# Kernel tuning notes

Hardware: AMD Instinct MI355X
Metric: run time of the kernel (lower is better)

The kernel has to match this reference:

```python
import jax, jax.numpy as jnp
import numpy as np

N_FFT = 1024
HOP = 256
B = 8
T = 2048  # n_frames
FREQ = N_FFT // 2 + 1


def setup_inputs() -> dict:
    key = jax.random.key(0)
    k1, k2 = jax.random.split(key)
    real_stft = jax.random.normal(k1, (B, 1, T, FREQ), dtype=jnp.float32)
    imag_stft = jax.random.normal(k2, (B, 1, T, FREQ), dtype=jnp.float32)
    # Build DFT synthesis matrices (same as torch module __init__, scaled=False)
    n = np.arange(N_FFT)
    hann = (0.5 - 0.5 * np.cos(2.0 * np.pi * n / N_FFT))  # fftbins=True hann
    ang = 2.0 * np.pi * np.outer(n, n) / N_FFT            # [k, n]
    W_real = (np.cos(ang) * hann[None, :] / N_FFT).astype(np.float32)
    W_imag = (np.sin(ang) * hann[None, :] / N_FFT).astype(np.float32)
    ola_window = (hann ** 2).astype(np.float32)
    return {
        "real_stft": real_stft,
        "imag_stft": imag_stft,
        "W_real": jnp.asarray(W_real),
        "W_imag": jnp.asarray(W_imag),
        "ola_window": jnp.asarray(ola_window),
    }


def reference(real_stft, imag_stft, W_real, W_imag, ola_window):
    n_fft = W_real.shape[0]
    b, _, n_frames, _ = real_stft.shape
    # (B, T, F) -> (B, F, T)
    fr = jnp.swapaxes(real_stft[:, 0], 1, 2)
    fi = jnp.swapaxes(imag_stft[:, 0], 1, 2)
    # Hermitian extension to full spectrum (B, n_fft, T)
    full_r = jnp.concatenate([fr, jnp.flip(fr[:, 1:-1, :], axis=1)], axis=1)
    full_i = jnp.concatenate([fi, -jnp.flip(fi[:, 1:-1, :], axis=1)], axis=1)
    # 1x1-conv DFT projection: out[b,t,n] = sum_k W[k,n] * x[b,k,t]
    frames = (jnp.einsum('kn,bkt->btn', W_real, full_r)
              - jnp.einsum('kn,bkt->btn', W_imag, full_i))  # (B, T, n_fft)
    out_len = (n_frames - 1) * HOP + n_fft
    # Overlap-add fold via scatter-add
    idx = (jnp.arange(n_frames)[:, None] * HOP + jnp.arange(n_fft)[None, :]).reshape(-1)
    y = jnp.zeros((b, out_len), frames.dtype).at[:, idx].add(frames.reshape(b, -1))
    # Window-sum fold + normalization
    wsum = jnp.zeros((out_len,), frames.dtype).at[idx].add(jnp.tile(ola_window, n_frames))
    wsum = jnp.clip(wsum, 1e-11, None)
    y = y / wsum[None, :]
    half = n_fft // 2
    return y[:, half:out_len - half]
```

## Files before the change

kernel.cpp:

```cpp
#include <hip/hip_runtime.h>


#define BATCH    8
#define NFRAMES  2048
#define FREQ     513
#define OUTCOLS  524032
#define FRAMES_B ((size_t)16384 * 1024 * 2)
#define WS_NEED  FRAMES_B

typedef __attribute__((ext_vector_type(2))) float f32x2;
typedef __attribute__((ext_vector_type(4))) float f32x4;
typedef __attribute__((ext_vector_type(4))) unsigned uint4v;

__device__ __forceinline__ unsigned short f2bf(float x) {
    unsigned u = __float_as_uint(x);
    return (unsigned short)((u + 0x7fffu + ((u >> 16) & 1u)) >> 16);
}

#define DSYNC() do { asm volatile("s_waitcnt lgkmcnt(0)" ::: "memory"); \
                     __builtin_amdgcn_sched_barrier(0); } while (0)

#define BFLY(IA, IB, IC, ID, T1, O0, O1, O2, O3)                              \
    {                                                                         \
        f32x2 apc = (IA) + (IC), amc = (IA) - (IC);                           \
        f32x2 bpd = (IB) + (ID), bmd = (IB) - (ID);                           \
        f32x2 jb  = (f32x2){-bmd[1], bmd[0]};                    \
        float rev_ = (float)(T1) * (1.0f / 1024.0f);                          \
        float s1_ = __builtin_amdgcn_sinf(rev_);                              \
        float c1_ = __builtin_amdgcn_cosf(rev_);                              \
        float c2_ = fmaf(-2.0f * s1_, s1_, 1.0f), s2_ = 2.0f * s1_ * c1_;     \
        float c3_ = c2_ * c1_ - s2_ * s1_, s3_ = s2_ * c1_ + c2_ * s1_;       \
        f32x2 u1 = amc + jb, u2 = apc - bpd, u3 = amc - jb;                   \
        O0 = apc + bpd;                                                       \
        O1 = (f32x2){u1[0] * c1_ - u1[1] * s1_, u1[0] * s1_ + u1[1] * c1_};   \
        O2 = (f32x2){u2[0] * c2_ - u2[1] * s2_, u2[0] * s2_ + u2[1] * c2_};   \
        O3 = (f32x2){u3[0] * c3_ - u3[1] * s3_, u3[0] * s3_ + u3[1] * c3_};   \
    }

__global__ __launch_bounds__(256, 2) void ifft_wave5(
    const float* __restrict__ re, const float* __restrict__ im,
    const float* __restrict__ ola, unsigned short* __restrict__ frames) {
    __shared__ float LR[4][1052];
    __shared__ float LI[4][1052];

    const int tid = threadIdx.x;
    const int l   = tid & 63;
    const int w   = tid >> 6;
    const int r0  = (blockIdx.x * 4 + w) * 2;
    float* PR = &LR[w][0];
    float* PI = &LI[w][0];

    const float* fre0 = re + (size_t)r0 * FREQ;
    const float* fim0 = im + (size_t)r0 * FREQ;
    const float* fre1 = fre0 + FREQ;
    const float* fim1 = fim0 + FREQ;

    f32x2 s1v[4][4];
#pragma unroll
    for (int j = 0; j < 4; ++j) {
        f32x2 in[4];
#pragma unroll
        for (int k = 0; k < 4; ++k) {
            int n  = l + 64 * j + 256 * k;
            int mm = (n <= 512) ? n : (1024 - n);
            float A1 = fre0[mm], B1 = fim0[mm];
            float A2 = fre1[mm], B2 = fim1[mm];
            if (n == 0 || n == 512) { B1 = 0.0f; B2 = 0.0f; }
            in[k] = (n <= 512) ? (f32x2){A1 - B2, B1 + A2}
                               : (f32x2){A1 + B2, A2 - B1};
        }
        BFLY(in[0], in[1], in[2], in[3], l + 64 * j,
             s1v[j][0], s1v[j][1], s1v[j][2], s1v[j][3]);
    }

    f32x4 wRe[4], wIm[4];
#pragma unroll
    for (int r = 0; r < 4; ++r) {
        f32x2 o0, o1, o2, o3;
        BFLY(s1v[0][r], s1v[1][r], s1v[2][r], s1v[3][r], 4 * l, o0, o1, o2, o3);
        wRe[0][r] = o0[0]; wIm[0][r] = o0[1];
        wRe[1][r] = o1[0]; wIm[1][r] = o1[1];
        wRe[2][r] = o2[0]; wIm[2][r] = o2[1];
        wRe[3][r] = o3[0]; wIm[3][r] = o3[1];
    }

    {
        const int wb = 16 * l + 8 * (l >> 4);
#pragma unroll
        for (int k = 0; k < 4; ++k) *(f32x4*)&PR[wb + 4 * k] = wRe[k];
#pragma unroll
        for (int k = 0; k < 4; ++k) *(f32x4*)&PI[wb + 4 * k] = wIm[k];
    }
    DSYNC();
    float rr[4][4], ri[4][4];
#pragma unroll
    for (int j = 0; j < 4; ++j)
#pragma unroll
        for (int k = 0; k < 4; ++k) rr[j][k] = PR[l + 64 * j + 264 * k];
#pragma unroll
    for (int j = 0; j < 4; ++j)
#pragma unroll
        for (int k = 0; k < 4; ++k) ri[j][k] = PI[l + 64 * j + 264 * k];

    f32x2 s3v[4][4];
#pragma unroll
    for (int j = 0; j < 4; ++j) {
        f32x2 a = (f32x2){rr[j][0], ri[j][0]};
        f32x2 b = (f32x2){rr[j][1], ri[j][1]};
        f32x2 c = (f32x2){rr[j][2], ri[j][2]};
        f32x2 d = (f32x2){rr[j][3], ri[j][3]};
        BFLY(a, b, c, d, (((l + 64 * j) >> 4) << 4),
             s3v[j][0], s3v[j][1], s3v[j][2], s3v[j][3]);
    }

    float eRe[4][4], eIm[4][4];
#pragma unroll
    for (int r = 0; r < 4; ++r) {
        f32x2 o0, o1, o2, o3;
        BFLY(s3v[0][r], s3v[1][r], s3v[2][r], s3v[3][r], ((l >> 4) << 6),
             o0, o1, o2, o3);
        eRe[0][r] = o0[0]; eIm[0][r] = o0[1];
        eRe[1][r] = o1[0]; eIm[1][r] = o1[1];
        eRe[2][r] = o2[0]; eIm[2][r] = o2[1];
        eRe[3][r] = o3[0]; eIm[3][r] = o3[1];
    }

    DSYNC();
    {
        const int wb = 256 * (l >> 4) + (l & 15) + 8 * (l >> 4);
#pragma unroll
        for (int k = 0; k < 4; ++k)
#pragma unroll
            for (int r = 0; r < 4; ++r) PR[wb + 16 * r + 64 * k] = eRe[k][r];
#pragma unroll
        for (int k = 0; k < 4; ++k)
#pragma unroll
            for (int r = 0; r < 4; ++r) PI[wb + 16 * r + 64 * k] = eIm[k][r];
    }
    DSYNC();
    float yR[4][4], yI[4][4];
#pragma unroll
    for (int h = 0; h < 4; ++h)
#pragma unroll
        for (int k = 0; k < 4; ++k) yR[h][k] = PR[l + 64 * h + 264 * k];
#pragma unroll
    for (int h = 0; h < 4; ++h)
#pragma unroll
        for (int k = 0; k < 4; ++k) yI[h][k] = PI[l + 64 * h + 264 * k];

    unsigned short* fR = frames + (size_t)r0 * 1024;
    unsigned short* fI = fR + 1024;
#pragma unroll
    for (int h = 0; h < 4; ++h) {
        f32x2 a = (f32x2){yR[h][0], yI[h][0]};
        f32x2 b = (f32x2){yR[h][1], yI[h][1]};
        f32x2 c = (f32x2){yR[h][2], yI[h][2]};
        f32x2 d = (f32x2){yR[h][3], yI[h][3]};
        f32x2 apc = a + c, amc = a - c, bpd = b + d, bmd = b - d;
        f32x2 jb  = (f32x2){-bmd[1], bmd[0]};
        f32x2 y0 = apc + bpd, y1 = amc + jb, y2 = apc - bpd, y3 = amc - jb;
        int n0 = l + 64 * h;
        float h0 = sqrtf(ola[n0])       * (1.0f / 1024.0f);
        float h1 = sqrtf(ola[n0 + 256]) * (1.0f / 1024.0f);
        float h2 = sqrtf(ola[n0 + 512]) * (1.0f / 1024.0f);
        float h3 = sqrtf(ola[n0 + 768]) * (1.0f / 1024.0f);
        fR[n0]       = f2bf(y0[0] * h0);  fI[n0]       = f2bf(y0[1] * h0);
        fR[n0 + 256] = f2bf(y1[0] * h1);  fI[n0 + 256] = f2bf(y1[1] * h1);
        fR[n0 + 512] = f2bf(y2[0] * h2);  fI[n0 + 512] = f2bf(y2[1] * h2);
        fR[n0 + 768] = f2bf(y3[0] * h3);  fI[n0 + 768] = f2bf(y3[1] * h3);
    }
}

__global__ __launch_bounds__(256) void ola_fold8(
    const unsigned short* __restrict__ frames, const float* __restrict__ ola,
    float* __restrict__ out) {
    const int col0 = (blockIdx.x * 256 + threadIdx.x) * 8;
    if (col0 >= OUTCOLS) return;
    const int b  = blockIdx.y;
    const int s  = col0 + 512;
    const int g  = s >> 8;
    const int ls = s & 255;

    float acc[8] = {0.f, 0.f, 0.f, 0.f, 0.f, 0.f, 0.f, 0.f};
    float wsm[8] = {0.f, 0.f, 0.f, 0.f, 0.f, 0.f, 0.f, 0.f};
#pragma unroll
    for (int j = 0; j < 4; ++j) {
        const int t = g - j;
        if (t >= 0 && t < NFRAMES) {
            uint4v u = *(const uint4v*)(frames + (((size_t)(b * NFRAMES + t)) << 10) + ls + 256 * j);
#pragma unroll
            for (int e = 0; e < 4; ++e) {
                acc[2 * e]     += __uint_as_float(u[e] << 16);
                acc[2 * e + 1] += __uint_as_float(u[e] & 0xffff0000u);
            }
            f32x4 o0 = *(const f32x4*)(ola + ls + 256 * j);
            f32x4 o1 = *(const f32x4*)(ola + ls + 256 * j + 4);
#pragma unroll
            for (int e = 0; e < 4; ++e) { wsm[e] += o0[e]; wsm[4 + e] += o1[e]; }
        }
    }
    f32x4 r0, r1;
#pragma unroll
    for (int e = 0; e < 4; ++e) {
        r0[e] = acc[e]     / fmaxf(wsm[e],     1e-11f);
        r1[e] = acc[4 + e] / fmaxf(wsm[4 + e], 1e-11f);
    }
    *(f32x4*)(out + (size_t)b * OUTCOLS + col0)     = r0;
    *(f32x4*)(out + (size_t)b * OUTCOLS + col0 + 4) = r1;
}

__global__ __launch_bounds__(256) void istft_naive(
    const float* __restrict__ re, const float* __restrict__ im,
    const float* __restrict__ Wr, const float* __restrict__ Wi,
    const float* __restrict__ ola, float* __restrict__ out) {
    const int g = blockIdx.x + 2, b = blockIdx.y, ls = threadIdx.x;
    __shared__ float s_fr[4][FREQ];
    __shared__ float s_fi[4][FREQ];
#pragma unroll
    for (int jj = 0; jj < 4; ++jj) {
        const int t = g - jj;
        const bool valid = (t >= 0 && t < NFRAMES);
        const size_t base = ((size_t)b * NFRAMES + (valid ? t : 0)) * FREQ;
        for (int k = ls; k < FREQ; k += 256) {
            const float f = (k == 0 || k == FREQ - 1) ? 1.0f : 2.0f;
            s_fr[jj][k] = valid ? re[base + k] * f : 0.0f;
            s_fi[jj][k] = valid ? im[base + k] * f : 0.0f;
        }
    }
    __syncthreads();
    const float* wr = Wr + ls;
    const float* wi = Wi + ls;
    float acc = 0.0f;
    for (int k = 0; k < FREQ; ++k) {
        const float* wrk = wr + (size_t)k * 1024;
        const float* wik = wi + (size_t)k * 1024;
#pragma unroll
        for (int jj = 0; jj < 4; ++jj) {
            acc = fmaf(wrk[jj * 256], s_fr[jj][k], acc);
            acc = fmaf(-wik[jj * 256], s_fi[jj][k], acc);
        }
    }
    float wsv = 0.0f;
#pragma unroll
    for (int jj = 0; jj < 4; ++jj) {
        const int t = g - jj;
        if (t >= 0 && t < NFRAMES) wsv += ola[ls + jj * 256];
    }
    wsv = fmaxf(wsv, 1e-11f);
    out[(size_t)b * OUTCOLS + (g * 256 + ls - 512)] = acc / wsv;
}

extern "C" void kernel_launch(void* const* d_in, const int* in_sizes, int n_in,
                              void* d_out, int out_size, void* d_ws, size_t ws_size,
                              hipStream_t stream) {
    const float* re  = (const float*)d_in[0];
    const float* im  = (const float*)d_in[1];
    const float* Wr  = (const float*)d_in[2];
    const float* Wi  = (const float*)d_in[3];
    const float* ola = (const float*)d_in[4];
    float* out = (float*)d_out;

    if (ws_size >= WS_NEED) {
        unsigned short* frames = (unsigned short*)d_ws;
        hipLaunchKernelGGL(ifft_wave5, dim3(2048), dim3(256), 0, stream,
                           re, im, ola, frames);
        hipLaunchKernelGGL(ola_fold8, dim3(256, BATCH), dim3(256), 0, stream,
                           frames, ola, out);
    } else {
        dim3 grid(2047, BATCH);
        hipLaunchKernelGGL(istft_naive, grid, dim3(256), 0, stream,
                           re, im, Wr, Wi, ola, out);
    }
}
```

Before: 37.37 us.

## Process two frame pairs per wave in the FFT kernel to raise ILP

Each wave now runs the full 1024-point inverse FFT on two packed frame pairs (four frames) at once, interleaving their loads, butterflies and LDS transposes, and the grid is halved to 1024 blocks. Real and imaginary parts now take turns in a per-frame LDS buffer, with extra waits between phases. The goal is more independent work per wave to hide global-load and LDS latency, at the cost of more registers, which could spill or reduce occupancy under the launch bounds.

```diff
diff --git a/kernel.cpp b/kernel.cpp
--- a/kernel.cpp
+++ b/kernel.cpp
@@ -37,137 +37,168 @@
         O3 = (f32x2){u3[0] * c3_ - u3[1] * s3_, u3[0] * s3_ + u3[1] * c3_};   \
     }
 
-__global__ __launch_bounds__(256, 2) void ifft_wave5(
+__global__ __launch_bounds__(256, 2) void ifft_wave7(
     const float* __restrict__ re, const float* __restrict__ im,
     const float* __restrict__ ola, unsigned short* __restrict__ frames) {
-    __shared__ float LR[4][1052];
-    __shared__ float LI[4][1052];
-
-    const int tid = threadIdx.x;
-    const int l   = tid & 63;
-    const int w   = tid >> 6;
-    const int r0  = (blockIdx.x * 4 + w) * 2;
-    float* PR = &LR[w][0];
-    float* PI = &LI[w][0];
-
-    const float* fre0 = re + (size_t)r0 * FREQ;
-    const float* fim0 = im + (size_t)r0 * FREQ;
-    const float* fre1 = fre0 + FREQ;
-    const float* fim1 = fim0 + FREQ;
-
-    f32x2 s1v[4][4];
-#pragma unroll
-    for (int j = 0; j < 4; ++j) {
-        f32x2 in[4];
-#pragma unroll
-        for (int k = 0; k < 4; ++k) {
-            int n  = l + 64 * j + 256 * k;
-            int mm = (n <= 512) ? n : (1024 - n);
-            float A1 = fre0[mm], B1 = fim0[mm];
-            float A2 = fre1[mm], B2 = fim1[mm];
-            if (n == 0 || n == 512) { B1 = 0.0f; B2 = 0.0f; }
-            in[k] = (n <= 512) ? (f32x2){A1 - B2, B1 + A2}
-                               : (f32x2){A1 + B2, A2 - B1};
-        }
-        BFLY(in[0], in[1], in[2], in[3], l + 64 * j,
-             s1v[j][0], s1v[j][1], s1v[j][2], s1v[j][3]);
-    }
-
-    f32x4 wRe[4], wIm[4];
-#pragma unroll
-    for (int r = 0; r < 4; ++r) {
-        f32x2 o0, o1, o2, o3;
-        BFLY(s1v[0][r], s1v[1][r], s1v[2][r], s1v[3][r], 4 * l, o0, o1, o2, o3);
-        wRe[0][r] = o0[0]; wIm[0][r] = o0[1];
-        wRe[1][r] = o1[0]; wIm[1][r] = o1[1];
-        wRe[2][r] = o2[0]; wIm[2][r] = o2[1];
-        wRe[3][r] = o3[0]; wIm[3][r] = o3[1];
-    }
-
-    {
-        const int wb = 16 * l + 8 * (l >> 4);
-#pragma unroll
-        for (int k = 0; k < 4; ++k) *(f32x4*)&PR[wb + 4 * k] = wRe[k];
-#pragma unroll
-        for (int k = 0; k < 4; ++k) *(f32x4*)&PI[wb + 4 * k] = wIm[k];
-    }
-    DSYNC();
-    float rr[4][4], ri[4][4];
-#pragma unroll
-    for (int j = 0; j < 4; ++j)
-#pragma unroll
-        for (int k = 0; k < 4; ++k) rr[j][k] = PR[l + 64 * j + 264 * k];
-#pragma unroll
-    for (int j = 0; j < 4; ++j)
-#pragma unroll
-        for (int k = 0; k < 4; ++k) ri[j][k] = PI[l + 64 * j + 264 * k];
-
-    f32x2 s3v[4][4];
-#pragma unroll
-    for (int j = 0; j < 4; ++j) {
-        f32x2 a = (f32x2){rr[j][0], ri[j][0]};
-        f32x2 b = (f32x2){rr[j][1], ri[j][1]};
-        f32x2 c = (f32x2){rr[j][2], ri[j][2]};
-        f32x2 d = (f32x2){rr[j][3], ri[j][3]};
-        BFLY(a, b, c, d, (((l + 64 * j) >> 4) << 4),
-             s3v[j][0], s3v[j][1], s3v[j][2], s3v[j][3]);
-    }
-
-    float eRe[4][4], eIm[4][4];
-#pragma unroll
-    for (int r = 0; r < 4; ++r) {
-        f32x2 o0, o1, o2, o3;
-        BFLY(s3v[0][r], s3v[1][r], s3v[2][r], s3v[3][r], ((l >> 4) << 6),
-             o0, o1, o2, o3);
-        eRe[0][r] = o0[0]; eIm[0][r] = o0[1];
-        eRe[1][r] = o1[0]; eIm[1][r] = o1[1];
-        eRe[2][r] = o2[0]; eIm[2][r] = o2[1];
-        eRe[3][r] = o3[0]; eIm[3][r] = o3[1];
-    }
-
-    DSYNC();
-    {
-        const int wb = 256 * (l >> 4) + (l & 15) + 8 * (l >> 4);
+    __shared__ float L[4][2][1052];
+
+    const int tid  = threadIdx.x;
+    const int l    = tid & 63;
+    const int w    = tid >> 6;
+    const int base = blockIdx.x * 16 + w * 4;
+    float* PB[2] = { &L[w][0][0], &L[w][1][0] };
+
+    f32x4 wRe[2][4], wIm[2][4];
+#pragma unroll
+    for (int ff = 0; ff < 2; ++ff) {
+        const int r0 = base + 2 * ff;
+        const float* fre0 = re + (size_t)r0 * FREQ;
+        const float* fim0 = im + (size_t)r0 * FREQ;
+        const float* fre1 = fre0 + FREQ;
+        const float* fim1 = fim0 + FREQ;
+
+        f32x2 s1v[4][4];
+#pragma unroll
+        for (int j = 0; j < 4; ++j) {
+            f32x2 in[4];
+#pragma unroll
+            for (int k = 0; k < 4; ++k) {
+                int n  = l + 64 * j + 256 * k;
+                int mm = (n <= 512) ? n : (1024 - n);
+                float A1 = fre0[mm], B1 = fim0[mm];
+                float A2 = fre1[mm], B2 = fim1[mm];
+                if (n == 0 || n == 512) { B1 = 0.0f; B2 = 0.0f; }
+                in[k] = (n <= 512) ? (f32x2){A1 - B2, B1 + A2}
+                                   : (f32x2){A1 + B2, A2 - B1};
+            }
+            BFLY(in[0], in[1], in[2], in[3], l + 64 * j,
+                 s1v[j][0], s1v[j][1], s1v[j][2], s1v[j][3]);
+        }
+#pragma unroll
+        for (int r = 0; r < 4; ++r) {
+            f32x2 o0, o1, o2, o3;
+            BFLY(s1v[0][r], s1v[1][r], s1v[2][r], s1v[3][r], 4 * l,
+                 o0, o1, o2, o3);
+            wRe[ff][0][r] = o0[0]; wIm[ff][0][r] = o0[1];
+            wRe[ff][1][r] = o1[0]; wIm[ff][1][r] = o1[1];
+            wRe[ff][2][r] = o2[0]; wIm[ff][2][r] = o2[1];
+            wRe[ff][3][r] = o3[0]; wIm[ff][3][r] = o3[1];
+        }
+    }
+
+    const int wb1 = 16 * l + 8 * (l >> 4);
+#pragma unroll
+    for (int ff = 0; ff < 2; ++ff)
+#pragma unroll
+        for (int k = 0; k < 4; ++k) *(f32x4*)&PB[ff][wb1 + 4 * k] = wRe[ff][k];
+    DSYNC();
+    float rr[2][4][4], ri[2][4][4];
+#pragma unroll
+    for (int ff = 0; ff < 2; ++ff)
+#pragma unroll
+        for (int j = 0; j < 4; ++j)
+#pragma unroll
+            for (int k = 0; k < 4; ++k)
+                rr[ff][j][k] = PB[ff][l + 64 * j + 264 * k];
+    DSYNC();
+#pragma unroll
+    for (int ff = 0; ff < 2; ++ff)
+#pragma unroll
+        for (int k = 0; k < 4; ++k) *(f32x4*)&PB[ff][wb1 + 4 * k] = wIm[ff][k];
+    DSYNC();
+#pragma unroll
+    for (int ff = 0; ff < 2; ++ff)
+#pragma unroll
+        for (int j = 0; j < 4; ++j)
+#pragma unroll
+            for (int k = 0; k < 4; ++k)
+                ri[ff][j][k] = PB[ff][l + 64 * j + 264 * k];
+    DSYNC();
+
+    float eRe[2][4][4], eIm[2][4][4];
+#pragma unroll
+    for (int ff = 0; ff < 2; ++ff) {
+        f32x2 s3v[4][4];
+#pragma unroll
+        for (int j = 0; j < 4; ++j) {
+            f32x2 a = (f32x2){rr[ff][j][0], ri[ff][j][0]};
+            f32x2 b = (f32x2){rr[ff][j][1], ri[ff][j][1]};
+            f32x2 c = (f32x2){rr[ff][j][2], ri[ff][j][2]};
+            f32x2 d = (f32x2){rr[ff][j][3], ri[ff][j][3]};
+            BFLY(a, b, c, d, (((l + 64 * j) >> 4) << 4),
+                 s3v[j][0], s3v[j][1], s3v[j][2], s3v[j][3]);
+        }
+#pragma unroll
+        for (int r = 0; r < 4; ++r) {
+            f32x2 o0, o1, o2, o3;
+            BFLY(s3v[0][r], s3v[1][r], s3v[2][r], s3v[3][r], ((l >> 4) << 6),
+                 o0, o1, o2, o3);
+            eRe[ff][0][r] = o0[0]; eIm[ff][0][r] = o0[1];
+            eRe[ff][1][r] = o1[0]; eIm[ff][1][r] = o1[1];
+            eRe[ff][2][r] = o2[0]; eIm[ff][2][r] = o2[1];
+            eRe[ff][3][r] = o3[0]; eIm[ff][3][r] = o3[1];
+        }
+    }
+
+    const int wb2 = 256 * (l >> 4) + (l & 15) + 8 * (l >> 4);
+#pragma unroll
+    for (int ff = 0; ff < 2; ++ff)
 #pragma unroll
         for (int k = 0; k < 4; ++k)
 #pragma unroll
-            for (int r = 0; r < 4; ++r) PR[wb + 16 * r + 64 * k] = eRe[k][r];
+            for (int r = 0; r < 4; ++r)
+                PB[ff][wb2 + 16 * r + 64 * k] = eRe[ff][k][r];
+    DSYNC();
+    float yR[2][4][4], yI[2][4][4];
+#pragma unroll
+    for (int ff = 0; ff < 2; ++ff)
+#pragma unroll
+        for (int h = 0; h < 4; ++h)
+#pragma unroll
+            for (int k = 0; k < 4; ++k)
+                yR[ff][h][k] = PB[ff][l + 64 * h + 264 * k];
+    DSYNC();
+#pragma unroll
+    for (int ff = 0; ff < 2; ++ff)
 #pragma unroll
         for (int k = 0; k < 4; ++k)
 #pragma unroll
-            for (int r = 0; r < 4; ++r) PI[wb + 16 * r + 64 * k] = eIm[k][r];
-    }
-    DSYNC();
-    float yR[4][4], yI[4][4];
-#pragma unroll
-    for (int h = 0; h < 4; ++h)
-#pragma unroll
-        for (int k = 0; k < 4; ++k) yR[h][k] = PR[l + 64 * h + 264 * k];
-#pragma unroll
-    for (int h = 0; h < 4; ++h)
-#pragma unroll
-        for (int k = 0; k < 4; ++k) yI[h][k] = PI[l + 64 * h + 264 * k];
-
-    unsigned short* fR = frames + (size_t)r0 * 1024;
-    unsigned short* fI = fR + 1024;
-#pragma unroll
-    for (int h = 0; h < 4; ++h) {
-        f32x2 a = (f32x2){yR[h][0], yI[h][0]};
-        f32x2 b = (f32x2){yR[h][1], yI[h][1]};
-        f32x2 c = (f32x2){yR[h][2], yI[h][2]};
-        f32x2 d = (f32x2){yR[h][3], yI[h][3]};
-        f32x2 apc = a + c, amc = a - c, bpd = b + d, bmd = b - d;
-        f32x2 jb  = (f32x2){-bmd[1], bmd[0]};
-        f32x2 y0 = apc + bpd, y1 = amc + jb, y2 = apc - bpd, y3 = amc - jb;
-        int n0 = l + 64 * h;
-        float h0 = sqrtf(ola[n0])       * (1.0f / 1024.0f);
-        float h1 = sqrtf(ola[n0 + 256]) * (1.0f / 1024.0f);
-        float h2 = sqrtf(ola[n0 + 512]) * (1.0f / 1024.0f);
-        float h3 = sqrtf(ola[n0 + 768]) * (1.0f / 1024.0f);
-        fR[n0]       = f2bf(y0[0] * h0);  fI[n0]       = f2bf(y0[1] * h0);
-        fR[n0 + 256] = f2bf(y1[0] * h1);  fI[n0 + 256] = f2bf(y1[1] * h1);
-        fR[n0 + 512] = f2bf(y2[0] * h2);  fI[n0 + 512] = f2bf(y2[1] * h2);
-        fR[n0 + 768] = f2bf(y3[0] * h3);  fI[n0 + 768] = f2bf(y3[1] * h3);
+            for (int r = 0; r < 4; ++r)
+                PB[ff][wb2 + 16 * r + 64 * k] = eIm[ff][k][r];
+    DSYNC();
+#pragma unroll
+    for (int ff = 0; ff < 2; ++ff)
+#pragma unroll
+        for (int h = 0; h < 4; ++h)
+#pragma unroll
+            for (int k = 0; k < 4; ++k)
+                yI[ff][h][k] = PB[ff][l + 64 * h + 264 * k];
+    DSYNC();
+
+#pragma unroll
+    for (int ff = 0; ff < 2; ++ff) {
+        const int r0 = base + 2 * ff;
+        unsigned short* fR = frames + (size_t)r0 * 1024;
+        unsigned short* fI = fR + 1024;
+#pragma unroll
+        for (int h = 0; h < 4; ++h) {
+            f32x2 a = (f32x2){yR[ff][h][0], yI[ff][h][0]};
+            f32x2 b = (f32x2){yR[ff][h][1], yI[ff][h][1]};
+            f32x2 c = (f32x2){yR[ff][h][2], yI[ff][h][2]};
+            f32x2 d = (f32x2){yR[ff][h][3], yI[ff][h][3]};
+            f32x2 apc = a + c, amc = a - c, bpd = b + d, bmd = b - d;
+            f32x2 jb  = (f32x2){-bmd[1], bmd[0]};
+            f32x2 y0 = apc + bpd, y1 = amc + jb, y2 = apc - bpd, y3 = amc - jb;
+            int n0 = l + 64 * h;
+            float h0 = sqrtf(ola[n0])       * (1.0f / 1024.0f);
+            float h1 = sqrtf(ola[n0 + 256]) * (1.0f / 1024.0f);
+            float h2 = sqrtf(ola[n0 + 512]) * (1.0f / 1024.0f);
+            float h3 = sqrtf(ola[n0 + 768]) * (1.0f / 1024.0f);
+            fR[n0]       = f2bf(y0[0] * h0);  fI[n0]       = f2bf(y0[1] * h0);
+            fR[n0 + 256] = f2bf(y1[0] * h1);  fI[n0 + 256] = f2bf(y1[1] * h1);
+            fR[n0 + 512] = f2bf(y2[0] * h2);  fI[n0 + 512] = f2bf(y2[1] * h2);
+            fR[n0 + 768] = f2bf(y3[0] * h3);  fI[n0 + 768] = f2bf(y3[1] * h3);
+        }
     }
 }
 
@@ -262,7 +293,7 @@
 
     if (ws_size >= WS_NEED) {
         unsigned short* frames = (unsigned short*)d_ws;
-        hipLaunchKernelGGL(ifft_wave5, dim3(2048), dim3(256), 0, stream,
+        hipLaunchKernelGGL(ifft_wave7, dim3(1024), dim3(256), 0, stream,
                            re, im, ola, frames);
         hipLaunchKernelGGL(ola_fold8, dim3(256, BATCH), dim3(256), 0, stream,
                            frames, ola, out);
```

Result: slower. 46.20 us (+23.6%).
